# Kernel optimization log

Hardware: AMD Instinct MI355X
Metric: run time of the kernel (lower is better)

Reference implementation:

```python
import jax, jax.numpy as jnp
import numpy as np
from functools import partial

B = 65536
IN_DIM, SEQ = 24, 40
N_KER, KSZ = 36, 3
ENC_DIM, HID, REG = 128, 64, 32
ODE_STEPS = 50  # fixed-step dopri5 (adaptive control replaced by fixed grid)

# Dormand-Prince 5(4) tableau (5th-order solution weights)
_A = [
    [1/5],
    [3/40, 9/40],
    [44/45, -56/15, 32/9],
    [19372/6561, -25360/2187, 64448/6561, -212/729],
    [9017/3168, -355/33, 46732/5247, 49/176, -5103/18656],
]
_BW = [35/384, 0.0, 500/1113, 125/192, -2187/6784, 11/84]


def _linear(x, W, b):
    return x @ W.T + b


def setup_inputs() -> dict:
    key = jax.random.key(0)
    ks = jax.random.split(key, 16)
    def w(k, shape, fan_in):
        lim = 1.0 / np.sqrt(fan_in)
        return jax.random.uniform(k, shape, jnp.float32, -lim, lim)
    return {
        "x": jax.random.normal(ks[0], (B, SEQ, IN_DIM), jnp.float32),
        "t_span": jnp.array([0.0, 1.0], jnp.float32),
        "conv_w": w(ks[1], (N_KER, IN_DIM, KSZ), IN_DIM * KSZ),
        "conv_b": w(ks[2], (N_KER,), IN_DIM * KSZ),
        "enc1_w": w(ks[3], (ENC_DIM, SEQ * N_KER), SEQ * N_KER),
        "enc1_b": w(ks[4], (ENC_DIM,), SEQ * N_KER),
        "enc2_w": w(ks[5], (HID, ENC_DIM), ENC_DIM),
        "enc2_b": w(ks[6], (HID,), ENC_DIM),
        "ode1_w": w(ks[7], (HID, HID), HID),
        "ode1_b": w(ks[8], (HID,), HID),
        "ode2_w": w(ks[9], (HID, HID), HID),
        "ode2_b": w(ks[10], (HID,), HID),
        "reg1_w": w(ks[11], (REG, HID), HID),
        "reg1_b": w(ks[12], (REG,), HID),
        "reg2_w": w(ks[13], (1, REG), REG),
        "reg2_b": w(ks[14], (1,), REG),
    }


def reference(x, t_span, conv_w, conv_b, enc1_w, enc1_b, enc2_w, enc2_b,
              ode1_w, ode1_b, ode2_w, ode2_b, reg1_w, reg1_b, reg2_w, reg2_b):
    # CNN: x [B,S,C] -> [B,C,S], Conv1d(pad=1) -> SiLU (dropout is eval no-op)
    h = jnp.transpose(x, (0, 2, 1))
    h = jax.lax.conv_general_dilated(
        h, conv_w, window_strides=(1,), padding=[(1, 1)],
        dimension_numbers=("NCH", "OIH", "NCH"))
    h = jax.nn.silu(h + conv_b[None, :, None])  # [B, N_KER, SEQ]
    # Encoder: Flatten (channel-major like torch) -> Linear -> ReLU -> Linear
    h = h.reshape(h.shape[0], -1)
    h = jax.nn.relu(_linear(h, enc1_w, enc1_b))
    theta0 = _linear(h, enc2_w, enc2_b)  # [B, HID]

    # Neural ODE RHS (assumed 2-layer tanh MLP, autonomous)
    def f(y):
        return _linear(jnp.tanh(_linear(y, ode1_w, ode1_b)), ode2_w, ode2_b)

    dt = (t_span[1] - t_span[0]) / ODE_STEPS

    def dopri5_step(y, _):
        k = [f(y)]
        for row in _A:
            yi = y + dt * sum(a * ki for a, ki in zip(row, k))
            k.append(f(yi))
        y_new = y + dt * sum(b * ki for b, ki in zip(_BW, k))
        return y_new, None

    theta_final, _ = jax.lax.scan(dopri5_step, theta0, None, length=ODE_STEPS)

    r = jax.nn.relu(_linear(theta_final, reg1_w, reg1_b))
    pred = _linear(r, reg2_w, reg2_b)
    return jnp.squeeze(pred, -1)  # [B]
```

## Files before the change

kernel.cpp:

```cpp
#include <hip/hip_runtime.h>
#include <hip/hip_bf16.h>

typedef __attribute__((ext_vector_type(8))) short short8;
typedef __attribute__((ext_vector_type(4))) float f32x4;

#define SEQ 40
#define IN_DIM 24
#define NKER 36
#define ENC 128
#define HID 64
#define NSTEPS 50
#define BTOT 65536

#define WS_FLAG 0
#define WS_DT   1
#define WS_CW   16
#define WS_CB   2608
#define WS_E1B  2644
#define WS_B1   2772
#define WS_CZ   2836
#define WS_CB2  2900
#define WS_R2W  2932
#define WS_R2B  2964
#define WS_EBZ  2976
#define WS_PB   3040
#define WS_BH   4096
#define WS_BL   106496
#define WS_EWZ  208896
#define WS_PW   217088
#define WS_MZH  221184
#define WS_MZL  223232
#define WS_QH   225280
#define WS_QL   226304
#define WS_ZP0  262144

__device__ __forceinline__ unsigned short f2bf(float f){
  union { float f; unsigned int u; } v; v.f = f;
  unsigned int r = (v.u + 0x7FFFu + ((v.u >> 16) & 1u)) >> 16;
  return (unsigned short)r;
}
__device__ __forceinline__ float bf2f(unsigned short s){
  union { unsigned int u; float f; } v; v.u = ((unsigned int)s) << 16; return v.f;
}
__device__ __forceinline__ float tanh_fast(float x){
  float ax = fabsf(x);
  float e  = __expf(-2.0f * ax);
  float t  = (1.0f - e) * __builtin_amdgcn_rcpf(1.0f + e);
  union { float f; unsigned int u; } vx, vt;
  vx.f = x; vt.f = t; vt.u |= (vx.u & 0x80000000u);
  return vt.f;
}

__global__ void k_detect(const void* __restrict__ x, const void* __restrict__ t_span,
                         float* __restrict__ ws){
  const unsigned int* xw = (const unsigned int*)x;
  int lane = threadIdx.x;
  int cnt = 0;
  #pragma unroll
  for (int i = 0; i < 16; i++){
    unsigned int w = xw[lane * 16 + i];
    unsigned int e = (w >> 7) & 0xFFu;
    cnt += (e >= 100u && e <= 140u) ? 1 : 0;
  }
  #pragma unroll
  for (int off = 32; off; off >>= 1) cnt += __shfl_down(cnt, off);
  if (lane == 0){
    int flag = (cnt >= 700) ? 1 : 0;
    float t0, t1;
    if (flag){
      t0 = __bfloat162float(((const __hip_bfloat16*)t_span)[0]);
      t1 = __bfloat162float(((const __hip_bfloat16*)t_span)[1]);
    } else {
      t0 = ((const float*)t_span)[0];
      t1 = ((const float*)t_span)[1];
    }
    ws[WS_FLAG] = (float)flag;
    ws[WS_DT] = (t1 - t0) / (float)NSTEPS;
  }
}

__global__ void k0_convert(const void* __restrict__ conv_w, const void* __restrict__ conv_b,
                           const void* __restrict__ enc1_w, const void* __restrict__ enc1_b,
                           const void* __restrict__ enc2_w, const void* __restrict__ enc2_b,
                           const void* __restrict__ ode1_w, const void* __restrict__ ode1_b,
                           const void* __restrict__ ode2_w, const void* __restrict__ ode2_b,
                           const void* __restrict__ reg1_w, const void* __restrict__ reg1_b,
                           const void* __restrict__ reg2_w, const void* __restrict__ reg2_b,
                           float* __restrict__ ws){
  const int flag = (int)ws[WS_FLAG];
  const float T = ws[WS_DT] * (float)NSTEPS;
  int t = blockIdx.x * 256 + threadIdx.x;
  int stride = gridDim.x * 256;

  #define RD(src, i) (flag ? __bfloat162float(((const __hip_bfloat16*)(src))[i]) \
                           : ((const float*)(src))[i])

  for (int i = t; i < NKER*72; i += stride){
    int o = i / 72, r = i % 72, dk = r / 24, c = r % 24;
    ws[WS_CW + i] = RD(conv_w, o*72 + c*3 + dk);
  }
  for (int i = t; i < NKER; i += stride) ws[WS_CB + i] = RD(conv_b, i);
  for (int i = t; i < ENC; i += stride) ws[WS_E1B + i] = RD(enc1_b, i);

  {
    unsigned short* bh = (unsigned short*)(ws + WS_BH);
    unsigned short* bl = (unsigned short*)(ws + WS_BL);
    for (int i = t; i < 8*50*64*8; i += stride){
      int j = i & 7, l = (i >> 3) & 63;
      int rem = i >> 9, ks = rem % 50, nt = rem / 50;
      int n = nt*16 + (l & 15);
      int kk = ks*32 + (l >> 4)*8 + j;
      int s = kk / 40, o = kk % 40;
      float v = (o < 36) ? RD(enc1_w, n*1440 + o*40 + s) : 0.0f;
      unsigned short h = f2bf(v);
      bh[i] = h; bl[i] = f2bf(v - bf2f(h));
    }
  }

  for (int i = t; i < 64*128; i += stride){
    int n = i >> 7, j = i & 127;
    float acc = 0.f;
    for (int h = 0; h < 64; h++) acc += RD(ode1_w, n*64+h) * RD(enc2_w, h*128+j);
    ws[WS_EWZ + i] = acc;
  }
  for (int i = t; i < 32*128; i += stride){
    int p = i >> 7, j = i & 127;
    float acc = 0.f;
    for (int h = 0; h < 64; h++) acc += RD(reg1_w, p*64+h) * RD(enc2_w, h*128+j);
    ws[WS_PW + i] = acc;
  }
  for (int i = t; i < 64; i += stride){
    float acc = 0.f;
    for (int h = 0; h < 64; h++) acc += RD(ode1_w, i*64+h) * RD(enc2_b, h);
    ws[WS_EBZ + i] = acc;
    float acc2 = 0.f;
    for (int h = 0; h < 64; h++) acc2 += RD(ode1_w, i*64+h) * RD(ode2_b, h);
    ws[WS_CZ + i] = acc2;
    ws[WS_B1 + i] = RD(ode1_b, i);
  }
  for (int i = t; i < 32; i += stride){
    float acc = 0.f;
    for (int h = 0; h < 64; h++) acc += RD(reg1_w, i*64+h) * RD(enc2_b, h);
    ws[WS_PB + i] = acc;
    float acc2 = 0.f;
    for (int h = 0; h < 64; h++) acc2 += RD(reg1_w, i*64+h) * RD(ode2_b, h);
    ws[WS_CB2 + i] = T * acc2 + RD(reg1_b, i);
    ws[WS_R2W + i] = RD(reg2_w, i);
  }
  if (t == 0) ws[WS_R2B] = RD(reg2_b, 0);

  unsigned short* mzh = (unsigned short*)(ws + WS_MZH);
  unsigned short* mzl = (unsigned short*)(ws + WS_MZL);
  for (int i = t; i < 64*64; i += stride){
    int a = i >> 6, b = i & 63;
    float acc = 0.f;
    for (int h = 0; h < 64; h++) acc += RD(ode1_w, a*64+h) * RD(ode2_w, h*64+b);
    unsigned short hi = f2bf(acc);
    mzh[i] = hi; mzl[i] = f2bf(acc - bf2f(hi));
  }
  unsigned short* qh = (unsigned short*)(ws + WS_QH);
  unsigned short* ql = (unsigned short*)(ws + WS_QL);
  for (int i = t; i < 32*64; i += stride){
    int p = i >> 6, b = i & 63;
    float acc = 0.f;
    for (int h = 0; h < 64; h++) acc += RD(reg1_w, p*64+h) * RD(ode2_w, h*64+b);
    unsigned short hi = f2bf(acc);
    qh[i] = hi; ql[i] = f2bf(acc - bf2f(hi));
  }
  #undef RD
}

__launch_bounds__(256, 4)
__global__ void k1_encoder(const void* __restrict__ x,
                           const float* __restrict__ ws,
                           float* __restrict__ zp0){
  __shared__ float lds[10240];
  unsigned short* Ahi = (unsigned short*)lds;
  unsigned short* Alo = Ahi + 64*160;
  const int flag = (int)ws[WS_FLAG];
  const int t = threadIdx.x;
  const int lane = t & 63;
  const int gu = __builtin_amdgcn_readfirstlane(t >> 6);
  const int wm = gu >> 1, wn = gu & 1;
  const int l15 = lane & 15, q = lane >> 4;
  const int r = lane;
  const long rowbase = (long)blockIdx.x * 64;

  f32x4 acc[2][4];
  #pragma unroll
  for (int mt = 0; mt < 2; mt++)
    #pragma unroll
    for (int nt = 0; nt < 4; nt++)
      acc[mt][nt] = (f32x4){0.f, 0.f, 0.f, 0.f};

  const unsigned short* BH = (const unsigned short*)(ws + WS_BH);
  const unsigned short* BL = (const unsigned short*)(ws + WS_BL);
  const float* CW = ws + WS_CW;
  const float* CB = ws + WS_CB;

  float xc[24];
  auto loadcol = [&](int col){
    if (col >= 0 && col < SEQ){
      if (flag){
        const __hip_bfloat16* xp = (const __hip_bfloat16*)x + (rowbase + r)*(SEQ*IN_DIM) + col*IN_DIM;
        const uint4* px = (const uint4*)xp;
        #pragma unroll
        for (int w8 = 0; w8 < 3; w8++){
          uint4 u = px[w8];
          unsigned int uu[4] = {u.x, u.y, u.z, u.w};
          #pragma unroll
          for (int e = 0; e < 4; e++){
            union { unsigned int i; float f; } lo, hi;
            lo.i = uu[e] << 16; hi.i = uu[e] & 0xffff0000u;
            xc[w8*8 + 2*e] = lo.f; xc[w8*8 + 2*e + 1] = hi.f;
          }
        }
      } else {
        const float* xp = (const float*)x + (rowbase + r)*(SEQ*IN_DIM) + col*IN_DIM;
        #pragma unroll
        for (int w4 = 0; w4 < 6; w4++){
          float4 v = ((const float4*)xp)[w4];
          xc[4*w4] = v.x; xc[4*w4+1] = v.y; xc[4*w4+2] = v.z; xc[4*w4+3] = v.w;
        }
      }
    } else {
      #pragma unroll
      for (int cc = 0; cc < 24; cc++) xc[cc] = 0.f;
    }
  };

  auto swzb = [](int blk, int rw){ return blk ^ ((blk < 16) ? (rw & 7) : (rw & 3)); };

  #pragma unroll 1
  for (int c = 0; c < 10; c++){
    __syncthreads();
    {
      const int s = c*4 + gu;
      float accv[36];
      #pragma unroll
      for (int o = 0; o < 36; o++) accv[o] = CB[o];
      #pragma unroll 1
      for (int dk = 0; dk < 3; dk++){
        loadcol(s - 1 + dk);
        const float* wdk = CW + dk*24;
        #pragma unroll
        for (int o = 0; o < 36; o++){
          const float* wo = wdk + o*72;
          float a = accv[o];
          #pragma unroll
          for (int ci = 0; ci < 24; ci++) a += wo[ci] * xc[ci];
          accv[o] = a;
        }
      }
      const int kb0 = gu * 40;
      #pragma unroll
      for (int o = 0; o < 40; o += 2){
        unsigned int hpack, lpack;
        if (o < 36){
          float v0 = accv[o];     v0 = v0 * __builtin_amdgcn_rcpf(1.0f + __expf(-v0));
          float v1 = accv[o + 1]; v1 = v1 * __builtin_amdgcn_rcpf(1.0f + __expf(-v1));
          unsigned short h0 = f2bf(v0), h1 = f2bf(v1);
          unsigned short l0 = f2bf(v0 - bf2f(h0)), l1 = f2bf(v1 - bf2f(h1));
          hpack = (unsigned int)h0 | ((unsigned int)h1 << 16);
          lpack = (unsigned int)l0 | ((unsigned int)l1 << 16);
        } else { hpack = 0u; lpack = 0u; }
        int k = kb0 + o;
        int idx = r*160 + (swzb(k >> 3, r) << 3) + (k & 7);
        *(unsigned int*)(Ahi + idx) = hpack;
        *(unsigned int*)(Alo + idx) = lpack;
      }
    }
    __syncthreads();
    #pragma unroll
    for (int ksl = 0; ksl < 5; ksl++){
      const int ks = c*5 + ksl;
      short8 ah[2], al[2];
      #pragma unroll
      for (int mt = 0; mt < 2; mt++){
        int rr = wm*32 + mt*16 + l15;
        int kb = ksl*4 + q;
        int idx = rr*160 + (swzb(kb, rr) << 3);
        ah[mt] = *(const short8*)(Ahi + idx);
        al[mt] = *(const short8*)(Alo + idx);
      }
      #pragma unroll
      for (int nt = 0; nt < 4; nt++){
        int fo = (((wn*4 + nt)*50 + ks)*64 + lane) << 3;
        short8 bh = *(const short8*)(BH + fo);
        short8 bl = *(const short8*)(BL + fo);
        #pragma unroll
        for (int mt = 0; mt < 2; mt++){
          acc[mt][nt] = __builtin_amdgcn_mfma_f32_16x16x32_bf16(ah[mt], bh, acc[mt][nt], 0, 0, 0);
          acc[mt][nt] = __builtin_amdgcn_mfma_f32_16x16x32_bf16(al[mt], bh, acc[mt][nt], 0, 0, 0);
          acc[mt][nt] = __builtin_amdgcn_mfma_f32_16x16x32_bf16(ah[mt], bl, acc[mt][nt], 0, 0, 0);
        }
      }
    }
  }

  __syncthreads();
  float* e1buf = lds;
  #pragma unroll
  for (int mt = 0; mt < 2; mt++){
    #pragma unroll
    for (int nt = 0; nt < 4; nt++){
      int col = wn*64 + nt*16 + l15;
      float bias = ws[WS_E1B + col];
      #pragma unroll
      for (int r2 = 0; r2 < 4; r2++){
        int row = wm*32 + mt*16 + q*4 + r2;
        float v = acc[mt][nt][r2] + bias;
        e1buf[row*129 + col] = v > 0.0f ? v : 0.0f;
      }
    }
  }
  __syncthreads();

  {
    const int n0 = gu * 24;
    float accs[24];
    #pragma unroll
    for (int i = 0; i < 24; i++){
      int n = n0 + i;
      accs[i] = (n < 64) ? ws[WS_EBZ + n] : ws[WS_PB + (n - 64)];
    }
    const float* e1r = e1buf + r*129;
    #pragma unroll 4
    for (int j = 0; j < 128; j++){
      float e = e1r[j];
      #pragma unroll
      for (int i = 0; i < 24; i++){
        int n = n0 + i;
        const float* wp = (n < 64) ? (ws + WS_EWZ + n*128) : (ws + WS_PW + (n - 64)*128);
        accs[i] += e * wp[j];
      }
    }
    float* dst = zp0 + (rowbase + r)*96 + n0;
    #pragma unroll
    for (int i = 0; i < 24; i += 4){
      f32x4 v = {accs[i], accs[i+1], accs[i+2], accs[i+3]};
      *(f32x4*)(dst + i) = v;
    }
  }
}

__launch_bounds__(64, 2)
__global__ void k2_ode(const float* __restrict__ ws,
                       const float* __restrict__ zp0,
                       float* __restrict__ out){
  __shared__ float scr[64*17];
  const int tid = threadIdx.x;
  const int l = tid & 15, q = tid >> 4;
  const int sl8 = 8 * ((l >> 2) & 1);
  const int rowbase = blockIdx.x * 16;

  short8 mh[2][4], ml[2][4];
  {
    const short8* pmh = (const short8*)(ws + WS_MZH);
    const short8* pml = (const short8*)(ws + WS_MZL);
    #pragma unroll
    for (int nt = 0; nt < 4; nt++){
      int n = nt*16 + l;
      #pragma unroll
      for (int kc = 0; kc < 2; kc++){
        int idx = n*8 + kc*4 + q;
        mh[kc][nt] = pmh[idx];
        ml[kc][nt] = pml[idx];
      }
    }
  }
  float b1v[4], czv[4];
  #pragma unroll
  for (int nt = 0; nt < 4; nt++){
    b1v[nt] = ws[WS_B1 + nt*16 + l];
    czv[nt] = ws[WS_CZ + nt*16 + l];
  }
  const float dt = ws[WS_DT];

  float z[16], s[16];
  #pragma unroll
  for (int i = 0; i < 16; i++){
    int nt = i >> 2, r = i & 3;
    z[i] = zp0[(long)(rowbase + q*4 + r) * 96 + nt*16 + l];
    s[i] = 0.0f;
  }

  auto put_tile = [&](const float* u){
    __syncthreads();
    #pragma unroll
    for (int nt = 0; nt < 4; nt++){
      int base = (nt*16 + l)*17 + ((q*4) ^ sl8);
      scr[base+0] = u[nt*4+0];
      scr[base+1] = u[nt*4+1];
      scr[base+2] = u[nt*4+2];
      scr[base+3] = u[nt*4+3];
    }
    __syncthreads();
  };
  auto get_frags = [&](short8& a0h, short8& a1h, short8& a0l, short8& a1l){
    union { short sv[8]; short8 v; } u0h, u1h, u0l, u1l;
    #pragma unroll
    for (int j = 0; j < 8; j++){
      int mp = (j < 4) ? l : (l ^ 8);
      float v0 = scr[(q*8 + j)*17 + mp];
      float v1 = scr[(q*8 + j + 32)*17 + mp];
      unsigned short h0 = f2bf(v0);
      unsigned short h1 = f2bf(v1);
      u0h.sv[j] = (short)h0; u0l.sv[j] = (short)f2bf(v0 - bf2f(h0));
      u1h.sv[j] = (short)h1; u1l.sv[j] = (short)f2bf(v1 - bf2f(h1));
    }
    a0h = u0h.v; a1h = u1h.v; a0l = u0l.v; a1l = u1l.v;
  };

  auto feval = [&](const float* v, float* g, float w){
    float u[16];
    #pragma unroll
    for (int nt = 0; nt < 4; nt++){
      #pragma unroll
      for (int r = 0; r < 4; r++) u[nt*4+r] = tanh_fast(v[nt*4+r] + b1v[nt]);
    }
    if (w != 0.0f){
      #pragma unroll
      for (int i = 0; i < 16; i++) s[i] += w * u[i];
    }
    put_tile(u);
    short8 a0h, a1h, a0l, a1l;
    get_frags(a0h, a1h, a0l, a1l);
    #pragma unroll
    for (int nt = 0; nt < 4; nt++){
      f32x4 c = {0.f, 0.f, 0.f, 0.f};
      c = __builtin_amdgcn_mfma_f32_16x16x32_bf16(a0h, mh[0][nt], c, 0, 0, 0);
      c = __builtin_amdgcn_mfma_f32_16x16x32_bf16(a1h, mh[1][nt], c, 0, 0, 0);
      c = __builtin_amdgcn_mfma_f32_16x16x32_bf16(a0l, mh[0][nt], c, 0, 0, 0);
      c = __builtin_amdgcn_mfma_f32_16x16x32_bf16(a1l, mh[1][nt], c, 0, 0, 0);
      c = __builtin_amdgcn_mfma_f32_16x16x32_bf16(a0h, ml[0][nt], c, 0, 0, 0);
      c = __builtin_amdgcn_mfma_f32_16x16x32_bf16(a1h, ml[1][nt], c, 0, 0, 0);
      #pragma unroll
      for (int r = 0; r < 4; r++) g[nt*4+r] = c[r] + czv[nt];
    }
  };

  const float c21 = dt * 0.2f;
  const float c31 = dt * (3.0f/40.0f),      c32 = dt * (9.0f/40.0f);
  const float c41 = dt * (44.0f/45.0f),     c42 = dt * (-56.0f/15.0f),   c43 = dt * (32.0f/9.0f);
  const float c51 = dt * (19372.0f/6561.0f), c52 = dt * (-25360.0f/2187.0f),
              c53 = dt * (64448.0f/6561.0f), c54 = dt * (-212.0f/729.0f);
  const float c61 = dt * (9017.0f/3168.0f),  c62 = dt * (-355.0f/33.0f),
              c63 = dt * (46732.0f/5247.0f), c64 = dt * (49.0f/176.0f),
              c65 = dt * (-5103.0f/18656.0f);
  const float d1 = dt * (35.0f/384.0f), d3 = dt * (500.0f/1113.0f), d4 = dt * (125.0f/192.0f),
              d5 = dt * (-2187.0f/6784.0f), d6 = dt * (11.0f/84.0f);

  float g1[16], g2[16], g3[16], g4[16], g5[16], g6[16], yt[16];

  #pragma unroll 1
  for (int st = 0; st < NSTEPS; st++){
    feval(z, g1, d1);
    #pragma unroll
    for (int i = 0; i < 16; i++) yt[i] = z[i] + c21*g1[i];
    feval(yt, g2, 0.0f);
    #pragma unroll
    for (int i = 0; i < 16; i++) yt[i] = z[i] + c31*g1[i] + c32*g2[i];
    feval(yt, g3, d3);
    #pragma unroll
    for (int i = 0; i < 16; i++) yt[i] = z[i] + c41*g1[i] + c42*g2[i] + c43*g3[i];
    feval(yt, g4, d4);
    #pragma unroll
    for (int i = 0; i < 16; i++) yt[i] = z[i] + c51*g1[i] + c52*g2[i] + c53*g3[i] + c54*g4[i];
    feval(yt, g5, d5);
    #pragma unroll
    for (int i = 0; i < 16; i++) yt[i] = z[i] + c61*g1[i] + c62*g2[i] + c63*g3[i] + c64*g4[i] + c65*g5[i];
    feval(yt, g6, d6);
    #pragma unroll
    for (int i = 0; i < 16; i++) z[i] = z[i] + d1*g1[i] + d3*g3[i] + d4*g4[i] + d5*g5[i] + d6*g6[i];
  }

  {
    put_tile(s);
    short8 a0h, a1h, a0l, a1l;
    get_frags(a0h, a1h, a0l, a1l);
    const short8* pqh = (const short8*)(ws + WS_QH);
    const short8* pql = (const short8*)(ws + WS_QL);
    float rr[2][4];
    #pragma unroll
    for (int nt2 = 0; nt2 < 2; nt2++){
      int n = nt2*16 + l;
      short8 qh0 = pqh[n*8 + q];
      short8 qh1 = pqh[n*8 + 4 + q];
      short8 ql0 = pql[n*8 + q];
      short8 ql1 = pql[n*8 + 4 + q];
      f32x4 c = {0.f, 0.f, 0.f, 0.f};
      c = __builtin_amdgcn_mfma_f32_16x16x32_bf16(a0h, qh0, c, 0, 0, 0);
      c = __builtin_amdgcn_mfma_f32_16x16x32_bf16(a1h, qh1, c, 0, 0, 0);
      c = __builtin_amdgcn_mfma_f32_16x16x32_bf16(a0l, qh0, c, 0, 0, 0);
      c = __builtin_amdgcn_mfma_f32_16x16x32_bf16(a1l, qh1, c, 0, 0, 0);
      c = __builtin_amdgcn_mfma_f32_16x16x32_bf16(a0h, ql0, c, 0, 0, 0);
      c = __builtin_amdgcn_mfma_f32_16x16x32_bf16(a1h, ql1, c, 0, 0, 0);
      float cbn = ws[WS_CB2 + n];
      #pragma unroll
      for (int r = 0; r < 4; r++){
        float p0 = zp0[(long)(rowbase + q*4 + r) * 96 + 64 + n];
        float v = c[r] + cbn + p0;
        rr[nt2][r] = v > 0.0f ? v : 0.0f;
      }
    }
    float w2v0 = ws[WS_R2W + l];
    float w2v1 = ws[WS_R2W + 16 + l];
    float part[4];
    #pragma unroll
    for (int r = 0; r < 4; r++) part[r] = rr[0][r]*w2v0 + rr[1][r]*w2v1;
    #pragma unroll
    for (int off = 1; off < 16; off <<= 1){
      #pragma unroll
      for (int r = 0; r < 4; r++) part[r] += __shfl_xor(part[r], off);
    }
    float r2b = ws[WS_R2B];
    if (l == 0){
      #pragma unroll
      for (int r = 0; r < 4; r++)
        out[rowbase + q*4 + r] = part[r] + r2b;
    }
  }
}

extern "C" void kernel_launch(void* const* d_in, const int* in_sizes, int n_in,
                              void* d_out, int out_size, void* d_ws, size_t ws_size,
                              hipStream_t stream){
  (void)in_sizes; (void)n_in; (void)out_size; (void)ws_size;
  float* ws = (float*)d_ws;

  k_detect<<<dim3(1), dim3(64), 0, stream>>>(d_in[0], d_in[1], ws);
  k0_convert<<<dim3(64), dim3(256), 0, stream>>>(
      d_in[2], d_in[3], d_in[4], d_in[5], d_in[6], d_in[7],
      d_in[8], d_in[9], d_in[10], d_in[11], d_in[12], d_in[13],
      d_in[14], d_in[15], ws);
  k1_encoder<<<dim3(BTOT/64), dim3(256), 0, stream>>>(d_in[0], ws, ws + WS_ZP0);
  k2_ode<<<dim3(BTOT/16), dim3(64), 0, stream>>>(ws, ws + WS_ZP0, (float*)d_out);
}
```

Measured before the change: 1.588 ms.

## Use MFMA for encoder projection, transpose ODE GEMM, and fold RK stage algebra

The encoder's final projection moves from a scalar FMA loop onto fp16 MFMA with a hi/lo split of weights and activations. The ODE kernel switches to a transposed layout, where the weight matrix is the A operand and the per-row state is B. This removes the barrier-based tile transpose and per-element bf16 splitting, replacing them with packed conversions and swizzled LDS writes. It also uses a cheaper tanh, and folds g2 into a combined term so one fewer stage buffer is kept live. The fp16 split and the cheaper tanh change numerical error, and the kernel relies on single-wave blocks to drop the syncthreads.

```diff
diff --git a/kernel.cpp b/kernel.cpp
--- a/kernel.cpp
+++ b/kernel.cpp
@@ -3,6 +3,8 @@
 
 typedef __attribute__((ext_vector_type(8))) short short8;
 typedef __attribute__((ext_vector_type(4))) float f32x4;
+typedef __attribute__((ext_vector_type(2))) __fp16 fp16x2;
+typedef __attribute__((ext_vector_type(8))) _Float16 half8;
 
 #define SEQ 40
 #define IN_DIM 24
@@ -26,12 +28,12 @@
 #define WS_PB   3040
 #define WS_BH   4096
 #define WS_BL   106496
-#define WS_EWZ  208896
-#define WS_PW   217088
 #define WS_MZH  221184
 #define WS_MZL  223232
 #define WS_QH   225280
 #define WS_QL   226304
+#define WS_EPWH 227328
+#define WS_EPWL 233472
 #define WS_ZP0  262144
 
 __device__ __forceinline__ unsigned short f2bf(float f){
@@ -42,13 +44,34 @@
 __device__ __forceinline__ float bf2f(unsigned short s){
   union { unsigned int u; float f; } v; v.u = ((unsigned int)s) << 16; return v.f;
 }
-__device__ __forceinline__ float tanh_fast(float x){
-  float ax = fabsf(x);
-  float e  = __expf(-2.0f * ax);
-  float t  = (1.0f - e) * __builtin_amdgcn_rcpf(1.0f + e);
-  union { float f; unsigned int u; } vx, vt;
-  vx.f = x; vt.f = t; vt.u |= (vx.u & 0x80000000u);
-  return vt.f;
+__device__ __forceinline__ unsigned int pk_bf16(float a, float b){
+  unsigned int r;
+  asm("v_cvt_pk_bf16_f32 %0, %1, %2" : "=v"(r) : "v"(a), "v"(b));
+  return r;
+}
+__device__ __forceinline__ void split_pair(float v0, float v1,
+                                           unsigned int& h, unsigned int& lo){
+  h = pk_bf16(v0, v1);
+  union { unsigned int u; float f; } a, b;
+  a.u = h << 16; b.u = h & 0xffff0000u;
+  lo = pk_bf16(v0 - a.f, v1 - b.f);
+}
+__device__ __forceinline__ unsigned int pk_f16(float a, float b){
+  fp16x2 h = __builtin_amdgcn_cvt_pkrtz(a, b);
+  union { fp16x2 h; unsigned int u; } cv; cv.h = h; return cv.u;
+}
+__device__ __forceinline__ float f16lo(unsigned int u){
+  union { unsigned short s; __fp16 h; } c; c.s = (unsigned short)(u & 0xffffu);
+  return (float)c.h;
+}
+__device__ __forceinline__ float f16hi(unsigned int u){
+  union { unsigned short s; __fp16 h; } c; c.s = (unsigned short)(u >> 16);
+  return (float)c.h;
+}
+__device__ __forceinline__ float tanh5(float x){
+  float e = __builtin_exp2f(x * 2.885390081777927f);
+  float r = __builtin_amdgcn_rcpf(1.0f + e);
+  return __builtin_fmaf(-2.0f, r, 1.0f);
 }
 
 __global__ void k_detect(const void* __restrict__ x, const void* __restrict__ t_span,
@@ -117,18 +140,28 @@
     }
   }
 
-  for (int i = t; i < 64*128; i += stride){
-    int n = i >> 7, j = i & 127;
-    float acc = 0.f;
-    for (int h = 0; h < 64; h++) acc += RD(ode1_w, n*64+h) * RD(enc2_w, h*128+j);
-    ws[WS_EWZ + i] = acc;
-  }
-  for (int i = t; i < 32*128; i += stride){
-    int p = i >> 7, j = i & 127;
-    float acc = 0.f;
-    for (int h = 0; h < 64; h++) acc += RD(reg1_w, p*64+h) * RD(enc2_w, h*128+j);
-    ws[WS_PW + i] = acc;
-  }
+  {
+    unsigned short* eph = (unsigned short*)(ws + WS_EPWH);
+    unsigned short* epl = (unsigned short*)(ws + WS_EPWL);
+    for (int i = t; i < 6*4*64*8; i += stride){
+      int j = i & 7, l = (i >> 3) & 63, kc = (i >> 9) & 3, nt = i >> 11;
+      int n = nt*16 + (l & 15);
+      int k = kc*32 + (l >> 4)*8 + j;
+      float acc = 0.f;
+      if (n < 64){
+        for (int h = 0; h < 64; h++) acc += RD(ode1_w, n*64+h) * RD(enc2_w, h*128+k);
+      } else {
+        int p = n - 64;
+        for (int h = 0; h < 64; h++) acc += RD(reg1_w, p*64+h) * RD(enc2_w, h*128+k);
+      }
+      unsigned int hp = pk_f16(acc, 0.f);
+      float hf = f16lo(hp);
+      unsigned int lp = pk_f16((acc - hf) * 2048.0f, 0.f);
+      eph[i] = (unsigned short)(hp & 0xffffu);
+      epl[i] = (unsigned short)(lp & 0xffffu);
+    }
+  }
+
   for (int i = t; i < 64; i += stride){
     float acc = 0.f;
     for (int h = 0; h < 64; h++) acc += RD(ode1_w, i*64+h) * RD(enc2_b, h);
@@ -259,10 +292,7 @@
         if (o < 36){
           float v0 = accv[o];     v0 = v0 * __builtin_amdgcn_rcpf(1.0f + __expf(-v0));
           float v1 = accv[o + 1]; v1 = v1 * __builtin_amdgcn_rcpf(1.0f + __expf(-v1));
-          unsigned short h0 = f2bf(v0), h1 = f2bf(v1);
-          unsigned short l0 = f2bf(v0 - bf2f(h0)), l1 = f2bf(v1 - bf2f(h1));
-          hpack = (unsigned int)h0 | ((unsigned int)h1 << 16);
-          lpack = (unsigned int)l0 | ((unsigned int)l1 << 16);
+          split_pair(v0, v1, hpack, lpack);
         } else { hpack = 0u; lpack = 0u; }
         int k = kb0 + o;
         int idx = r*160 + (swzb(k >> 3, r) << 3) + (k & 7);
@@ -310,36 +340,53 @@
       for (int r2 = 0; r2 < 4; r2++){
         int row = wm*32 + mt*16 + q*4 + r2;
         float v = acc[mt][nt][r2] + bias;
-        e1buf[row*129 + col] = v > 0.0f ? v : 0.0f;
+        e1buf[row*132 + col] = v > 0.0f ? v : 0.0f;
       }
     }
   }
   __syncthreads();
 
   {
-    const int n0 = gu * 24;
-    float accs[24];
-    #pragma unroll
-    for (int i = 0; i < 24; i++){
-      int n = n0 + i;
-      accs[i] = (n < 64) ? ws[WS_EBZ + n] : ws[WS_PB + (n - 64)];
-    }
-    const float* e1r = e1buf + r*129;
-    #pragma unroll 4
-    for (int j = 0; j < 128; j++){
-      float e = e1r[j];
-      #pragma unroll
-      for (int i = 0; i < 24; i++){
-        int n = n0 + i;
-        const float* wp = (n < 64) ? (ws + WS_EWZ + n*128) : (ws + WS_PW + (n - 64)*128);
-        accs[i] += e * wp[j];
-      }
-    }
-    float* dst = zp0 + (rowbase + r)*96 + n0;
-    #pragma unroll
-    for (int i = 0; i < 24; i += 4){
-      f32x4 v = {accs[i], accs[i+1], accs[i+2], accs[i+3]};
-      *(f32x4*)(dst + i) = v;
+    half8 eh[4], el[4];
+    const int myrow = gu*16 + l15;
+    #pragma unroll
+    for (int kc = 0; kc < 4; kc++){
+      const float* ep = e1buf + myrow*132 + kc*32 + q*8;
+      f32x4 va = *(const f32x4*)(ep);
+      f32x4 vb = *(const f32x4*)(ep + 4);
+      float v[8] = {va[0],va[1],va[2],va[3],vb[0],vb[1],vb[2],vb[3]};
+      union { unsigned int u[4]; half8 h8; } H, L;
+      #pragma unroll
+      for (int p = 0; p < 4; p++){
+        unsigned int h = pk_f16(v[2*p], v[2*p+1]);
+        float r0 = v[2*p]   - f16lo(h);
+        float r1 = v[2*p+1] - f16hi(h);
+        H.u[p] = h;
+        L.u[p] = pk_f16(r0, r1);
+      }
+      eh[kc] = H.h8; el[kc] = L.h8;
+    }
+    const unsigned short* EPH = (const unsigned short*)(ws + WS_EPWH);
+    const unsigned short* EPL = (const unsigned short*)(ws + WS_EPWL);
+    #pragma unroll 1
+    for (int nt = 0; nt < 6; nt++){
+      f32x4 c1 = (f32x4){0.f,0.f,0.f,0.f};
+      f32x4 c2 = (f32x4){0.f,0.f,0.f,0.f};
+      #pragma unroll
+      for (int kc = 0; kc < 4; kc++){
+        int fo = (((nt*4 + kc)*64 + lane)) << 3;
+        half8 bh = *(const half8*)(EPH + fo);
+        half8 bl = *(const half8*)(EPL + fo);
+        c1 = __builtin_amdgcn_mfma_f32_16x16x32_f16(eh[kc], bh, c1, 0, 0, 0);
+        c1 = __builtin_amdgcn_mfma_f32_16x16x32_f16(el[kc], bh, c1, 0, 0, 0);
+        c2 = __builtin_amdgcn_mfma_f32_16x16x32_f16(eh[kc], bl, c2, 0, 0, 0);
+      }
+      float bias = (nt < 4) ? ws[WS_EBZ + nt*16 + l15] : ws[WS_PB + (nt-4)*16 + l15];
+      #pragma unroll
+      for (int rr = 0; rr < 4; rr++){
+        zp0[(long)(rowbase + gu*16 + q*4 + rr)*96 + nt*16 + l15]
+            = c1[rr] + c2[rr]*(1.0f/2048.0f) + bias;
+      }
     }
   }
 }
@@ -348,178 +395,168 @@
 __global__ void k2_ode(const float* __restrict__ ws,
                        const float* __restrict__ zp0,
                        float* __restrict__ out){
-  __shared__ float scr[64*17];
+  __shared__ unsigned int scr[1152];
+  unsigned int* Uh = scr;
+  unsigned int* Ul = scr + 576;
   const int tid = threadIdx.x;
-  const int l = tid & 15, q = tid >> 4;
-  const int sl8 = 8 * ((l >> 2) & 1);
+  const int l15 = tid & 15, q = tid >> 4;
+  const int hswz = (l15 & 1) << 4;
   const int rowbase = blockIdx.x * 16;
 
-  short8 mh[2][4], ml[2][4];
+  short8 Ah[4][2], Al[4][2];
   {
     const short8* pmh = (const short8*)(ws + WS_MZH);
     const short8* pml = (const short8*)(ws + WS_MZL);
     #pragma unroll
-    for (int nt = 0; nt < 4; nt++){
-      int n = nt*16 + l;
+    for (int mt = 0; mt < 4; mt++)
       #pragma unroll
       for (int kc = 0; kc < 2; kc++){
-        int idx = n*8 + kc*4 + q;
-        mh[kc][nt] = pmh[idx];
-        ml[kc][nt] = pml[idx];
-      }
-    }
-  }
-  float b1v[4], czv[4];
+        int idx = (mt*16 + l15)*8 + kc*4 + q;
+        Ah[mt][kc] = pmh[idx];
+        Al[mt][kc] = pml[idx];
+      }
+  }
+  float b1a[16], cza[16];
   #pragma unroll
-  for (int nt = 0; nt < 4; nt++){
-    b1v[nt] = ws[WS_B1 + nt*16 + l];
-    czv[nt] = ws[WS_CZ + nt*16 + l];
+  for (int mt = 0; mt < 4; mt++){
+    f32x4 b  = *(const f32x4*)(ws + WS_B1 + mt*16 + q*4);
+    f32x4 cz = *(const f32x4*)(ws + WS_CZ + mt*16 + q*4);
+    #pragma unroll
+    for (int rr = 0; rr < 4; rr++){ b1a[mt*4+rr] = b[rr]; cza[mt*4+rr] = cz[rr]; }
   }
   const float dt = ws[WS_DT];
 
   float z[16], s[16];
   #pragma unroll
-  for (int i = 0; i < 16; i++){
-    int nt = i >> 2, r = i & 3;
-    z[i] = zp0[(long)(rowbase + q*4 + r) * 96 + nt*16 + l];
-    s[i] = 0.0f;
-  }
-
-  auto put_tile = [&](const float* u){
-    __syncthreads();
-    #pragma unroll
-    for (int nt = 0; nt < 4; nt++){
-      int base = (nt*16 + l)*17 + ((q*4) ^ sl8);
-      scr[base+0] = u[nt*4+0];
-      scr[base+1] = u[nt*4+1];
-      scr[base+2] = u[nt*4+2];
-      scr[base+3] = u[nt*4+3];
-    }
-    __syncthreads();
+  for (int mt = 0; mt < 4; mt++){
+    f32x4 v = *(const f32x4*)(zp0 + (long)(rowbase + l15)*96 + mt*16 + q*4);
+    #pragma unroll
+    for (int rr = 0; rr < 4; rr++){ z[mt*4+rr] = v[rr]; s[mt*4+rr] = 0.0f; }
+  }
+
+  const int wbase = l15*36;
+
+  auto feval = [&](const float* in, float* g, float w){
+    float u[16];
+    #pragma unroll
+    for (int i = 0; i < 16; i++) u[i] = tanh5(in[i] + b1a[i]);
+    if (w != 0.0f){
+      #pragma unroll
+      for (int i = 0; i < 16; i++) s[i] += w * u[i];
+    }
+    #pragma unroll
+    for (int mt = 0; mt < 4; mt++){
+      unsigned int h01, lo01, h23, lo23;
+      split_pair(u[mt*4+0], u[mt*4+1], h01, lo01);
+      split_pair(u[mt*4+2], u[mt*4+3], h23, lo23);
+      int slot = wbase + ((8*mt + 2*q) ^ hswz);
+      *(uint2*)(Uh + slot) = make_uint2(h01, h23);
+      *(uint2*)(Ul + slot) = make_uint2(lo01, lo23);
+    }
+    f32x4 c[4];
+    #pragma unroll
+    for (int mt = 0; mt < 4; mt++) c[mt] = (f32x4){0.f,0.f,0.f,0.f};
+    #pragma unroll
+    for (int kc = 0; kc < 2; kc++){
+      int rb = wbase + ((16*kc + 4*q) ^ hswz);
+      short8 bh = *(const short8*)(Uh + rb);
+      short8 bl = *(const short8*)(Ul + rb);
+      #pragma unroll
+      for (int mt = 0; mt < 4; mt++){
+        c[mt] = __builtin_amdgcn_mfma_f32_16x16x32_bf16(Ah[mt][kc], bh, c[mt], 0, 0, 0);
+        c[mt] = __builtin_amdgcn_mfma_f32_16x16x32_bf16(Al[mt][kc], bh, c[mt], 0, 0, 0);
+        c[mt] = __builtin_amdgcn_mfma_f32_16x16x32_bf16(Ah[mt][kc], bl, c[mt], 0, 0, 0);
+      }
+    }
+    #pragma unroll
+    for (int i = 0; i < 16; i++) g[i] = c[i>>2][i&3] + cza[i];
   };
-  auto get_frags = [&](short8& a0h, short8& a1h, short8& a0l, short8& a1l){
-    union { short sv[8]; short8 v; } u0h, u1h, u0l, u1l;
-    #pragma unroll
-    for (int j = 0; j < 8; j++){
-      int mp = (j < 4) ? l : (l ^ 8);
-      float v0 = scr[(q*8 + j)*17 + mp];
-      float v1 = scr[(q*8 + j + 32)*17 + mp];
-      unsigned short h0 = f2bf(v0);
-      unsigned short h1 = f2bf(v1);
-      u0h.sv[j] = (short)h0; u0l.sv[j] = (short)f2bf(v0 - bf2f(h0));
-      u1h.sv[j] = (short)h1; u1l.sv[j] = (short)f2bf(v1 - bf2f(h1));
-    }
-    a0h = u0h.v; a1h = u1h.v; a0l = u0l.v; a1l = u1l.v;
-  };
-
-  auto feval = [&](const float* v, float* g, float w){
-    float u[16];
-    #pragma unroll
-    for (int nt = 0; nt < 4; nt++){
-      #pragma unroll
-      for (int r = 0; r < 4; r++) u[nt*4+r] = tanh_fast(v[nt*4+r] + b1v[nt]);
-    }
-    if (w != 0.0f){
-      #pragma unroll
-      for (int i = 0; i < 16; i++) s[i] += w * u[i];
-    }
-    put_tile(u);
-    short8 a0h, a1h, a0l, a1l;
-    get_frags(a0h, a1h, a0l, a1l);
-    #pragma unroll
-    for (int nt = 0; nt < 4; nt++){
-      f32x4 c = {0.f, 0.f, 0.f, 0.f};
-      c = __builtin_amdgcn_mfma_f32_16x16x32_bf16(a0h, mh[0][nt], c, 0, 0, 0);
-      c = __builtin_amdgcn_mfma_f32_16x16x32_bf16(a1h, mh[1][nt], c, 0, 0, 0);
-      c = __builtin_amdgcn_mfma_f32_16x16x32_bf16(a0l, mh[0][nt], c, 0, 0, 0);
-      c = __builtin_amdgcn_mfma_f32_16x16x32_bf16(a1l, mh[1][nt], c, 0, 0, 0);
-      c = __builtin_amdgcn_mfma_f32_16x16x32_bf16(a0h, ml[0][nt], c, 0, 0, 0);
-      c = __builtin_amdgcn_mfma_f32_16x16x32_bf16(a1h, ml[1][nt], c, 0, 0, 0);
-      #pragma unroll
-      for (int r = 0; r < 4; r++) g[nt*4+r] = c[r] + czv[nt];
-    }
-  };
 
   const float c21 = dt * 0.2f;
-  const float c31 = dt * (3.0f/40.0f),      c32 = dt * (9.0f/40.0f);
-  const float c41 = dt * (44.0f/45.0f),     c42 = dt * (-56.0f/15.0f),   c43 = dt * (32.0f/9.0f);
-  const float c51 = dt * (19372.0f/6561.0f), c52 = dt * (-25360.0f/2187.0f),
-              c53 = dt * (64448.0f/6561.0f), c54 = dt * (-212.0f/729.0f);
-  const float c61 = dt * (9017.0f/3168.0f),  c62 = dt * (-355.0f/33.0f),
-              c63 = dt * (46732.0f/5247.0f), c64 = dt * (49.0f/176.0f),
+  const float c31 = dt * (3.0f/40.0f),  c32 = dt * (9.0f/40.0f);
+  const float c43 = dt * (32.0f/9.0f);
+  const float c53 = dt * (64448.0f/6561.0f), c54 = dt * (-212.0f/729.0f);
+  const float c63 = dt * (46732.0f/5247.0f), c64 = dt * (49.0f/176.0f),
               c65 = dt * (-5103.0f/18656.0f);
+  const float r42 = -448.0f/27.0f,          c41p = dt * (20.0f/9.0f);
+  const float r52 = -1014400.0f/19683.0f,   c51p = dt * (134196.0f/19683.0f);
+  const float r62 = -14200.0f/297.0f,       c61p = dt * (9017.0f/3168.0f + 42600.0f/11880.0f);
   const float d1 = dt * (35.0f/384.0f), d3 = dt * (500.0f/1113.0f), d4 = dt * (125.0f/192.0f),
               d5 = dt * (-2187.0f/6784.0f), d6 = dt * (11.0f/84.0f);
 
-  float g1[16], g2[16], g3[16], g4[16], g5[16], g6[16], yt[16];
+  float g1[16], A[16], g3[16], g4[16], g5[16], yt[16];
 
   #pragma unroll 1
   for (int st = 0; st < NSTEPS; st++){
     feval(z, g1, d1);
     #pragma unroll
     for (int i = 0; i < 16; i++) yt[i] = z[i] + c21*g1[i];
-    feval(yt, g2, 0.0f);
-    #pragma unroll
-    for (int i = 0; i < 16; i++) yt[i] = z[i] + c31*g1[i] + c32*g2[i];
+    feval(yt, A, 0.0f);
+    #pragma unroll
+    for (int i = 0; i < 16; i++){
+      A[i]  = c31*g1[i] + c32*A[i];
+      yt[i] = z[i] + A[i];
+    }
     feval(yt, g3, d3);
     #pragma unroll
-    for (int i = 0; i < 16; i++) yt[i] = z[i] + c41*g1[i] + c42*g2[i] + c43*g3[i];
+    for (int i = 0; i < 16; i++) yt[i] = z[i] + r42*A[i] + c41p*g1[i] + c43*g3[i];
     feval(yt, g4, d4);
     #pragma unroll
-    for (int i = 0; i < 16; i++) yt[i] = z[i] + c51*g1[i] + c52*g2[i] + c53*g3[i] + c54*g4[i];
+    for (int i = 0; i < 16; i++) yt[i] = z[i] + r52*A[i] + c51p*g1[i] + c53*g3[i] + c54*g4[i];
     feval(yt, g5, d5);
     #pragma unroll
-    for (int i = 0; i < 16; i++) yt[i] = z[i] + c61*g1[i] + c62*g2[i] + c63*g3[i] + c64*g4[i] + c65*g5[i];
-    feval(yt, g6, d6);
-    #pragma unroll
-    for (int i = 0; i < 16; i++) z[i] = z[i] + d1*g1[i] + d3*g3[i] + d4*g4[i] + d5*g5[i] + d6*g6[i];
+    for (int i = 0; i < 16; i++) yt[i] = z[i] + r62*A[i] + c61p*g1[i] + c63*g3[i] + c64*g4[i] + c65*g5[i];
+    feval(yt, A, d6);
+    #pragma unroll
+    for (int i = 0; i < 16; i++) z[i] += d1*g1[i] + d3*g3[i] + d4*g4[i] + d5*g5[i] + d6*A[i];
   }
 
   {
-    put_tile(s);
-    short8 a0h, a1h, a0l, a1l;
-    get_frags(a0h, a1h, a0l, a1l);
+    #pragma unroll
+    for (int mt = 0; mt < 4; mt++){
+      unsigned int h01, lo01, h23, lo23;
+      split_pair(s[mt*4+0], s[mt*4+1], h01, lo01);
+      split_pair(s[mt*4+2], s[mt*4+3], h23, lo23);
+      int slot = wbase + ((8*mt + 2*q) ^ hswz);
+      *(uint2*)(Uh + slot) = make_uint2(h01, h23);
+      *(uint2*)(Ul + slot) = make_uint2(lo01, lo23);
+    }
     const short8* pqh = (const short8*)(ws + WS_QH);
     const short8* pql = (const short8*)(ws + WS_QL);
-    float rr[2][4];
-    #pragma unroll
-    for (int nt2 = 0; nt2 < 2; nt2++){
-      int n = nt2*16 + l;
-      short8 qh0 = pqh[n*8 + q];
-      short8 qh1 = pqh[n*8 + 4 + q];
-      short8 ql0 = pql[n*8 + q];
-      short8 ql1 = pql[n*8 + 4 + q];
-      f32x4 c = {0.f, 0.f, 0.f, 0.f};
-      c = __builtin_amdgcn_mfma_f32_16x16x32_bf16(a0h, qh0, c, 0, 0, 0);
-      c = __builtin_amdgcn_mfma_f32_16x16x32_bf16(a1h, qh1, c, 0, 0, 0);
-      c = __builtin_amdgcn_mfma_f32_16x16x32_bf16(a0l, qh0, c, 0, 0, 0);
-      c = __builtin_amdgcn_mfma_f32_16x16x32_bf16(a1l, qh1, c, 0, 0, 0);
-      c = __builtin_amdgcn_mfma_f32_16x16x32_bf16(a0h, ql0, c, 0, 0, 0);
-      c = __builtin_amdgcn_mfma_f32_16x16x32_bf16(a1h, ql1, c, 0, 0, 0);
-      float cbn = ws[WS_CB2 + n];
-      #pragma unroll
-      for (int r = 0; r < 4; r++){
-        float p0 = zp0[(long)(rowbase + q*4 + r) * 96 + 64 + n];
-        float v = c[r] + cbn + p0;
-        rr[nt2][r] = v > 0.0f ? v : 0.0f;
-      }
-    }
-    float w2v0 = ws[WS_R2W + l];
-    float w2v1 = ws[WS_R2W + 16 + l];
-    float part[4];
-    #pragma unroll
-    for (int r = 0; r < 4; r++) part[r] = rr[0][r]*w2v0 + rr[1][r]*w2v1;
-    #pragma unroll
-    for (int off = 1; off < 16; off <<= 1){
-      #pragma unroll
-      for (int r = 0; r < 4; r++) part[r] += __shfl_xor(part[r], off);
-    }
-    float r2b = ws[WS_R2B];
-    if (l == 0){
-      #pragma unroll
-      for (int r = 0; r < 4; r++)
-        out[rowbase + q*4 + r] = part[r] + r2b;
-    }
+    f32x4 cv[2];
+    cv[0] = (f32x4){0.f,0.f,0.f,0.f};
+    cv[1] = (f32x4){0.f,0.f,0.f,0.f};
+    #pragma unroll
+    for (int kc = 0; kc < 2; kc++){
+      int rb = wbase + ((16*kc + 4*q) ^ hswz);
+      short8 bh = *(const short8*)(Uh + rb);
+      short8 bl = *(const short8*)(Ul + rb);
+      #pragma unroll
+      for (int mt2 = 0; mt2 < 2; mt2++){
+        int idx = (mt2*16 + l15)*8 + kc*4 + q;
+        short8 qh = pqh[idx];
+        short8 qlf = pql[idx];
+        cv[mt2] = __builtin_amdgcn_mfma_f32_16x16x32_bf16(qh,  bh, cv[mt2], 0, 0, 0);
+        cv[mt2] = __builtin_amdgcn_mfma_f32_16x16x32_bf16(qlf, bh, cv[mt2], 0, 0, 0);
+        cv[mt2] = __builtin_amdgcn_mfma_f32_16x16x32_bf16(qh,  bl, cv[mt2], 0, 0, 0);
+      }
+    }
+    float part = 0.f;
+    #pragma unroll
+    for (int mt2 = 0; mt2 < 2; mt2++){
+      f32x4 cb = *(const f32x4*)(ws + WS_CB2 + mt2*16 + q*4);
+      f32x4 p0 = *(const f32x4*)(zp0 + (long)(rowbase + l15)*96 + 64 + mt2*16 + q*4);
+      f32x4 w2 = *(const f32x4*)(ws + WS_R2W + mt2*16 + q*4);
+      #pragma unroll
+      for (int rr = 0; rr < 4; rr++){
+        float v = cv[mt2][rr] + cb[rr] + p0[rr];
+        v = v > 0.0f ? v : 0.0f;
+        part += w2[rr] * v;
+      }
+    }
+    part += __shfl_xor(part, 16);
+    part += __shfl_xor(part, 32);
+    if (q == 0) out[rowbase + l15] = part + ws[WS_R2B];
   }
 }
 
```

Result: slower. 2.490 ms (+56.8%).
